# Performance work log

Measured on AMD Instinct MI355X. Metric: run time of the kernel, lower is better.

## Reference

```python
import jax, jax.numpy as jnp
import numpy as np

N = 50000      # nodes
E = 800000     # edges (before self-loops)
IN_DIM = 128
HID = 96
PROJ = 64
BN_EPS = 1e-5
L2_EPS = 1e-12


def setup_inputs() -> dict:
    key = jax.random.key(0)
    ks = jax.random.split(key, 8)

    def glorot(k, shape):
        fan_in, fan_out = shape
        s = np.sqrt(6.0 / (fan_in + fan_out)).astype(np.float32)
        return jax.random.uniform(k, shape, jnp.float32, -s, s)

    x = jax.random.normal(ks[0], (N, IN_DIM), jnp.float32)
    edge_index = jax.random.randint(ks[1], (2, E), 0, N, dtype=jnp.int64)

    return {
        "x": x,
        "edge_index": edge_index,
        # GCN layer 1
        "W1": glorot(ks[2], (IN_DIM, HID)), "b1": jnp.zeros(HID, jnp.float32),
        "g1": jnp.ones(HID, jnp.float32), "be1": jnp.zeros(HID, jnp.float32),
        # GCN layer 2
        "W2": glorot(ks[3], (HID, HID)), "b2": jnp.zeros(HID, jnp.float32),
        "g2": jnp.ones(HID, jnp.float32), "be2": jnp.zeros(HID, jnp.float32),
        # projector: Linear -> BN -> ReLU -> Linear
        "Wp1": glorot(ks[4], (HID, HID)), "bp1": jnp.zeros(HID, jnp.float32),
        "gp": jnp.ones(HID, jnp.float32), "bep": jnp.zeros(HID, jnp.float32),
        "Wp2": glorot(ks[5], (HID, PROJ)), "bp2": jnp.zeros(PROJ, jnp.float32),
    }


def _batchnorm(h, gamma, beta):
    # training-mode BatchNorm1d: batch stats, biased variance
    m = h.mean(axis=0)
    v = h.var(axis=0)
    return gamma * (h - m) * jax.lax.rsqrt(v + BN_EPS) + beta


def _gcn_conv(x, W, b, src, dst, deg_inv_sqrt):
    # PyG GCNConv: x @ W, symmetric-normalized scatter-add (self-loops included
    # in src/dst), then bias.
    xw = x @ W                                              # [N, out]
    norm = deg_inv_sqrt[src] * deg_inv_sqrt[dst]            # [E+N]
    msg = xw[src] * norm[:, None]                           # [E+N, out]
    out = jax.ops.segment_sum(msg, dst, num_segments=x.shape[0])
    return out + b


def reference(x, edge_index, W1, b1, g1, be1, W2, b2, g2, be2,
              Wp1, bp1, gp, bep, Wp2, bp2):
    n = x.shape[0]
    loops = jnp.arange(n, dtype=edge_index.dtype)
    src = jnp.concatenate([edge_index[0], loops])
    dst = jnp.concatenate([edge_index[1], loops])
    deg = jax.ops.segment_sum(jnp.ones(src.shape[0], x.dtype), dst,
                              num_segments=n)               # includes self-loops
    deg_inv_sqrt = jax.lax.rsqrt(deg)                       # deg >= 1 always

    h = jax.nn.relu(_batchnorm(_gcn_conv(x, W1, b1, src, dst, deg_inv_sqrt), g1, be1))
    h = jax.nn.relu(_batchnorm(_gcn_conv(h, W2, b2, src, dst, deg_inv_sqrt), g2, be2))

    z = jax.nn.relu(_batchnorm(h @ Wp1 + bp1, gp, bep))
    z = z @ Wp2 + bp2
    # F.normalize(p=2, dim=-1, eps=1e-12)
    nrm = jnp.linalg.norm(z, axis=-1, keepdims=True)
    return z / jnp.maximum(nrm, L2_EPS)
```

## Files before the change

kernel.cpp:

```cpp
#include <hip/hip_runtime.h>
#include <hip/hip_fp16.h>

constexpr int BLK = 256;

static inline int cdiv(long long a, int b) { return (int)((a + b - 1) / b); }

using v8h = __attribute__((ext_vector_type(8))) _Float16;
using v4f = __attribute__((ext_vector_type(4))) float;


__global__ void count_dst_off(const int* __restrict__ dst, int* __restrict__ cnt,
                              unsigned short* __restrict__ eoff, int E) {
    for (int i = blockIdx.x * blockDim.x + threadIdx.x; i < E; i += gridDim.x * blockDim.x)
        eoff[i] = (unsigned short)atomicAdd(&cnt[dst[i]], 1);
}

__global__ __launch_bounds__(256) void scan1_dis(const int* __restrict__ cnt,
                                                 int* __restrict__ rowptr,
                                                 int* __restrict__ bsum,
                                                 float* __restrict__ dis, int N) {
    __shared__ int ts[256];
    int tid = threadIdx.x;
    int base = blockIdx.x * 1024 + tid * 4;
    int v[4], s = 0;
#pragma unroll
    for (int i = 0; i < 4; ++i) {
        v[i] = (base + i < N) ? cnt[base + i] : 0;
        s += v[i];
        if (base + i < N) dis[base + i] = rsqrtf((float)v[i] + 1.0f);
    }
    ts[tid] = s;
    __syncthreads();
    for (int off = 1; off < 256; off <<= 1) {
        int t = 0;
        if (tid >= off) t = ts[tid - off];
        __syncthreads();
        if (tid >= off) ts[tid] += t;
        __syncthreads();
    }
    int run = ts[tid] - s;
#pragma unroll
    for (int i = 0; i < 4; ++i) {
        if (base + i < N) rowptr[base + i] = run;
        run += v[i];
    }
    if (tid == 255) bsum[blockIdx.x] = ts[255];
}

__global__ __launch_bounds__(256) void scan23(int* __restrict__ rowptr,
                                              const int* __restrict__ bsum,
                                              int nb, int N, int E) {
    __shared__ int sboff[64];
    const int tid = threadIdx.x;
    if (tid < 64) {
        int orig = (tid < nb) ? bsum[tid] : 0;
        int v = orig;
#pragma unroll
        for (int off = 1; off < 64; off <<= 1) {
            int t = __shfl_up(v, off, 64);
            if (tid >= off) v += t;
        }
        sboff[tid] = v - orig;
    }
    __syncthreads();
    int i = blockIdx.x * 256 + tid;
    if (i < N) rowptr[i] += sboff[i >> 10];
    if (i == 0) rowptr[N] = E;
}

__global__ void csr_fill(const int* __restrict__ src, const int* __restrict__ dst,
                         const unsigned short* __restrict__ eoff,
                         const int* __restrict__ rowptr,
                         unsigned short* __restrict__ csrc, int E) {
    for (int i = blockIdx.x * blockDim.x + threadIdx.x; i < E; i += gridDim.x * blockDim.x) {
        csrc[rowptr[dst[i]] + (int)eoff[i]] = (unsigned short)src[i];
    }
}


template <int K, bool ACT, bool BIAS, bool HOUT, bool WOUT, bool STATS>
__device__ __forceinline__ void gemm96_body(int bid,
                                            const float* __restrict__ in,
                                            const float* __restrict__ W,
                                            const float* __restrict__ bias,
                                            const float* __restrict__ bnsums,
                                            const float* __restrict__ gamma,
                                            const float* __restrict__ beta,
                                            const float* __restrict__ dsc,
                                            float* __restrict__ out,
                                            _Float16* __restrict__ hout,
                                            float* __restrict__ osums, int N) {
    constexpr int NK = K / 32;
    constexpr int LDK = K + 8;
    __shared__ __align__(16) _Float16 Wt[96 * LDK];
    __shared__ __align__(16) float ssl[ACT ? 192 : 1];
    __shared__ float sb[STATS ? 192 : 1];
    const int tid = threadIdx.x;
    for (int idx = tid; idx < K * 96; idx += 256) {
        int k = idx / 96, n = idx - k * 96;
        Wt[n * LDK + k] = (_Float16)W[idx];
    }
    if (ACT && tid < 96) {
        float inv_n = 1.0f / (float)N;
        float mean = bnsums[tid] * inv_n;
        float var = bnsums[96 + tid] * inv_n - mean * mean;
        float sc = gamma[tid] * rsqrtf(var + 1e-5f);
        ssl[tid] = sc;
        ssl[96 + tid] = beta[tid] - mean * sc;
    }
    if (STATS && tid < 192) sb[tid] = 0.0f;
    __syncthreads();

    const int wave = tid >> 6, lane = tid & 63;
    const int quad = lane >> 4, lm = lane & 15;
    const int rbase = bid * 64 + wave * 16;
    int arow = rbase + lm;
    arow = arow < N ? arow : N - 1;

    v8h afr[NK];
#pragma unroll
    for (int kc = 0; kc < NK; ++kc) {
        const float* p = &in[(long long)arow * K + kc * 32 + quad * 8];
        float4 p0 = *(const float4*)p;
        float4 p1 = *(const float4*)(p + 4);
        if (ACT) {
            int kk = kc * 32 + quad * 8;
            float4 sc0 = *(const float4*)&ssl[kk];
            float4 sc1 = *(const float4*)&ssl[kk + 4];
            float4 sh0 = *(const float4*)&ssl[96 + kk];
            float4 sh1 = *(const float4*)&ssl[96 + kk + 4];
            p0.x = fmaxf(fmaf(p0.x, sc0.x, sh0.x), 0.0f);
            p0.y = fmaxf(fmaf(p0.y, sc0.y, sh0.y), 0.0f);
            p0.z = fmaxf(fmaf(p0.z, sc0.z, sh0.z), 0.0f);
            p0.w = fmaxf(fmaf(p0.w, sc0.w, sh0.w), 0.0f);
            p1.x = fmaxf(fmaf(p1.x, sc1.x, sh1.x), 0.0f);
            p1.y = fmaxf(fmaf(p1.y, sc1.y, sh1.y), 0.0f);
            p1.z = fmaxf(fmaf(p1.z, sc1.z, sh1.z), 0.0f);
            p1.w = fmaxf(fmaf(p1.w, sc1.w, sh1.w), 0.0f);
        }
        v8h a;
        a[0] = (_Float16)p0.x; a[1] = (_Float16)p0.y;
        a[2] = (_Float16)p0.z; a[3] = (_Float16)p0.w;
        a[4] = (_Float16)p1.x; a[5] = (_Float16)p1.y;
        a[6] = (_Float16)p1.z; a[7] = (_Float16)p1.w;
        afr[kc] = a;
    }

    v4f acc[6];
#pragma unroll
    for (int t = 0; t < 6; ++t) {
        v4f c = {0.0f, 0.0f, 0.0f, 0.0f};
#pragma unroll
        for (int kc = 0; kc < NK; ++kc) {
            v8h b = *(const v8h*)&Wt[(t * 16 + lm) * LDK + kc * 32 + quad * 8];
            c = __builtin_amdgcn_mfma_f32_16x16x32_f16(afr[kc], b, c, 0, 0, 0);
        }
        acc[t] = c;
    }

    float dr[4];
    if (HOUT) {
#pragma unroll
        for (int r = 0; r < 4; ++r) {
            int gr = rbase + quad * 4 + r;
            dr[r] = dsc ? dsc[gr < N ? gr : N - 1] : 1.0f;
        }
    }

    float ls[6], lq[6];
#pragma unroll
    for (int t = 0; t < 6; ++t) { ls[t] = 0.0f; lq[t] = 0.0f; }
#pragma unroll
    for (int t = 0; t < 6; ++t) {
        float bv = BIAS ? bias[t * 16 + lm] : 0.0f;
#pragma unroll
        for (int r = 0; r < 4; ++r) {
            int gr = rbase + quad * 4 + r;
            if (gr < N) {
                float o = acc[t][r] + bv;
                if (WOUT) out[(long long)gr * 96 + t * 16 + lm] = o;
                if (HOUT) hout[(long long)gr * 96 + t * 16 + lm] = (_Float16)(o * dr[r]);
                if (STATS) { ls[t] += o; lq[t] += o * o; }
            }
        }
    }
    if (STATS) {
#pragma unroll
        for (int t = 0; t < 6; ++t) {
            ls[t] += __shfl_xor(ls[t], 16);
            ls[t] += __shfl_xor(ls[t], 32);
            lq[t] += __shfl_xor(lq[t], 16);
            lq[t] += __shfl_xor(lq[t], 32);
        }
        if (quad == 0) {
#pragma unroll
            for (int t = 0; t < 6; ++t) {
                atomicAdd(&sb[t * 16 + lm], ls[t]);
                atomicAdd(&sb[96 + t * 16 + lm], lq[t]);
            }
        }
        __syncthreads();
        if (tid < 192) atomicAdd(&osums[tid], sb[tid]);
    }
}

template <int K, bool ACT, bool BIAS, bool HOUT, bool WOUT, bool STATS>
__global__ __launch_bounds__(256) void gemm96m(const float* __restrict__ in,
                                               const float* __restrict__ W,
                                               const float* __restrict__ bias,
                                               const float* __restrict__ bnsums,
                                               const float* __restrict__ gamma,
                                               const float* __restrict__ beta,
                                               const float* __restrict__ dsc,
                                               float* __restrict__ out,
                                               _Float16* __restrict__ hout,
                                               float* __restrict__ osums, int N) {
    gemm96_body<K, ACT, BIAS, HOUT, WOUT, STATS>(blockIdx.x, in, W, bias, bnsums,
                                                 gamma, beta, dsc, out, hout, osums, N);
}

__global__ __launch_bounds__(256) void gemm1_zero(const float* __restrict__ x,
                                                  const float* __restrict__ W1,
                                                  _Float16* __restrict__ hout,
                                                  int* __restrict__ cnt,
                                                  float* __restrict__ sums,
                                                  int gG, int N) {
    if ((int)blockIdx.x < gG) {
        gemm96_body<128, false, false, true, false, false>(
            blockIdx.x, x, W1, nullptr, nullptr, nullptr, nullptr, nullptr,
            nullptr, hout, nullptr, N);
    } else {
        int g = (blockIdx.x - gG) * 256 + threadIdx.x;
        int stride = (gridDim.x - gG) * 256;
        for (int i = g; i < N; i += stride) cnt[i] = 0;
        if (g < 576) sums[g] = 0.0f;
    }
}


__global__ __launch_bounds__(256) void gemm_finalm(const float* __restrict__ in,
                                                   const float* __restrict__ W,
                                                   const float* __restrict__ bias,
                                                   const float* __restrict__ bnsums,
                                                   const float* __restrict__ gamma,
                                                   const float* __restrict__ beta,
                                                   float* __restrict__ out, int N) {
    constexpr int K = 96, NK = 3, LDK = K + 8;
    __shared__ __align__(16) _Float16 Wt[64 * LDK];
    __shared__ __align__(16) float ssl[192];
    const int tid = threadIdx.x;
    for (int idx = tid; idx < K * 64; idx += 256) {
        int k = idx / 64, n = idx - k * 64;
        Wt[n * LDK + k] = (_Float16)W[idx];
    }
    if (tid < 96) {
        float inv_n = 1.0f / (float)N;
        float mean = bnsums[tid] * inv_n;
        float var = bnsums[96 + tid] * inv_n - mean * mean;
        float sc = gamma[tid] * rsqrtf(var + 1e-5f);
        ssl[tid] = sc;
        ssl[96 + tid] = beta[tid] - mean * sc;
    }
    __syncthreads();

    const int wave = tid >> 6, lane = tid & 63;
    const int quad = lane >> 4, lm = lane & 15;
    const int rbase = blockIdx.x * 64 + wave * 16;
    int arow = rbase + lm;
    arow = arow < N ? arow : N - 1;

    v8h afr[NK];
#pragma unroll
    for (int kc = 0; kc < NK; ++kc) {
        const float* p = &in[(long long)arow * K + kc * 32 + quad * 8];
        float4 p0 = *(const float4*)p;
        float4 p1 = *(const float4*)(p + 4);
        int kk = kc * 32 + quad * 8;
        float4 sc0 = *(const float4*)&ssl[kk];
        float4 sc1 = *(const float4*)&ssl[kk + 4];
        float4 sh0 = *(const float4*)&ssl[96 + kk];
        float4 sh1 = *(const float4*)&ssl[96 + kk + 4];
        p0.x = fmaxf(fmaf(p0.x, sc0.x, sh0.x), 0.0f);
        p0.y = fmaxf(fmaf(p0.y, sc0.y, sh0.y), 0.0f);
        p0.z = fmaxf(fmaf(p0.z, sc0.z, sh0.z), 0.0f);
        p0.w = fmaxf(fmaf(p0.w, sc0.w, sh0.w), 0.0f);
        p1.x = fmaxf(fmaf(p1.x, sc1.x, sh1.x), 0.0f);
        p1.y = fmaxf(fmaf(p1.y, sc1.y, sh1.y), 0.0f);
        p1.z = fmaxf(fmaf(p1.z, sc1.z, sh1.z), 0.0f);
        p1.w = fmaxf(fmaf(p1.w, sc1.w, sh1.w), 0.0f);
        v8h a;
        a[0] = (_Float16)p0.x; a[1] = (_Float16)p0.y;
        a[2] = (_Float16)p0.z; a[3] = (_Float16)p0.w;
        a[4] = (_Float16)p1.x; a[5] = (_Float16)p1.y;
        a[6] = (_Float16)p1.z; a[7] = (_Float16)p1.w;
        afr[kc] = a;
    }

    v4f acc[4];
#pragma unroll
    for (int t = 0; t < 4; ++t) {
        v4f c = {0.0f, 0.0f, 0.0f, 0.0f};
#pragma unroll
        for (int kc = 0; kc < NK; ++kc) {
            v8h b = *(const v8h*)&Wt[(t * 16 + lm) * LDK + kc * 32 + quad * 8];
            c = __builtin_amdgcn_mfma_f32_16x16x32_f16(afr[kc], b, c, 0, 0, 0);
        }
        float bv = bias[t * 16 + lm];
        c[0] += bv; c[1] += bv; c[2] += bv; c[3] += bv;
        acc[t] = c;
    }

    float sq[4];
#pragma unroll
    for (int r = 0; r < 4; ++r) {
        float s = acc[0][r] * acc[0][r] + acc[1][r] * acc[1][r] +
                  acc[2][r] * acc[2][r] + acc[3][r] * acc[3][r];
#pragma unroll
        for (int m = 1; m < 16; m <<= 1) s += __shfl_xor(s, m, 64);
        sq[r] = 1.0f / fmaxf(sqrtf(s), 1e-12f);
    }
#pragma unroll
    for (int r = 0; r < 4; ++r) {
        int gr = rbase + quad * 4 + r;
        if (gr < N) {
#pragma unroll
            for (int t = 0; t < 4; ++t)
                out[(long long)gr * 64 + t * 16 + lm] = acc[t][r] * sq[r];
        }
    }
}


__device__ __forceinline__ void acc_row(float* acc, const __half2* h) {
#pragma unroll
    for (int k = 0; k < 4; ++k) {
        float2 f = __half22float2(h[k]);
        acc[2 * k + 0] += f.x;
        acc[2 * k + 1] += f.y;
    }
}

__device__ __forceinline__ void acc_roww(float* acc, const __half2* h, float w) {
#pragma unroll
    for (int k = 0; k < 4; ++k) {
        float2 f = __half22float2(h[k]);
        acc[2 * k + 0] = fmaf(f.x, w, acc[2 * k + 0]);
        acc[2 * k + 1] = fmaf(f.y, w, acc[2 * k + 1]);
    }
}

template <bool PRESC>
__global__ __launch_bounds__(256) void agg96h(const __half* __restrict__ hxw,
                                              const int* __restrict__ rowptr,
                                              const unsigned short* __restrict__ csrc,
                                              const float* __restrict__ dis,
                                              const float* __restrict__ bias,
                                              float* __restrict__ out, int N) {
    int idx = blockIdx.x * 256 + threadIdx.x;
    if (idx >= N * 12) return;
    int n = idx / 12, c8 = idx % 12;
    int ch = c8 * 8;
    float dn = dis[n];
    float acc[8];
    {
        float sw = PRESC ? 1.0f : dn;
        float4 g = *(const float4*)&hxw[(long long)n * 96 + ch];
        const __half2* hs = (const __half2*)&g;
#pragma unroll
        for (int k = 0; k < 4; ++k) {
            float2 f = __half22float2(hs[k]);
            acc[2 * k + 0] = f.x * sw;
            acc[2 * k + 1] = f.y * sw;
        }
    }
    int e = rowptr[n], e1 = rowptr[n + 1];
    for (; e + 7 < e1; e += 8) {
        int s[8];
        float4 g[8];
        float w[8];
#pragma unroll
        for (int j = 0; j < 8; ++j) s[j] = csrc[e + j];
        if (!PRESC) {
#pragma unroll
            for (int j = 0; j < 8; ++j) w[j] = dis[s[j]];
        }
#pragma unroll
        for (int j = 0; j < 8; ++j)
            g[j] = *(const float4*)&hxw[(long long)s[j] * 96 + ch];
#pragma unroll
        for (int j = 0; j < 8; ++j) {
            if (PRESC) acc_row(acc, (const __half2*)&g[j]);
            else       acc_roww(acc, (const __half2*)&g[j], w[j]);
        }
    }
    for (; e + 3 < e1; e += 4) {
        int s[4];
        float4 g[4];
        float w[4];
#pragma unroll
        for (int j = 0; j < 4; ++j) s[j] = csrc[e + j];
        if (!PRESC) {
#pragma unroll
            for (int j = 0; j < 4; ++j) w[j] = dis[s[j]];
        }
#pragma unroll
        for (int j = 0; j < 4; ++j)
            g[j] = *(const float4*)&hxw[(long long)s[j] * 96 + ch];
#pragma unroll
        for (int j = 0; j < 4; ++j) {
            if (PRESC) acc_row(acc, (const __half2*)&g[j]);
            else       acc_roww(acc, (const __half2*)&g[j], w[j]);
        }
    }
    for (; e < e1; ++e) {
        int s0 = csrc[e];
        float4 g0 = *(const float4*)&hxw[(long long)s0 * 96 + ch];
        if (PRESC) acc_row(acc, (const __half2*)&g0);
        else       acc_roww(acc, (const __half2*)&g0, dis[s0]);
    }
    float4 o0, o1;
    o0.x = fmaf(acc[0], dn, bias[ch + 0]);
    o0.y = fmaf(acc[1], dn, bias[ch + 1]);
    o0.z = fmaf(acc[2], dn, bias[ch + 2]);
    o0.w = fmaf(acc[3], dn, bias[ch + 3]);
    o1.x = fmaf(acc[4], dn, bias[ch + 4]);
    o1.y = fmaf(acc[5], dn, bias[ch + 5]);
    o1.z = fmaf(acc[6], dn, bias[ch + 6]);
    o1.w = fmaf(acc[7], dn, bias[ch + 7]);
    *(float4*)&out[(long long)n * 96 + ch] = o0;
    *(float4*)&out[(long long)n * 96 + ch + 4] = o1;
}


__global__ __launch_bounds__(256) void bn_stats96(const float* __restrict__ h,
                                                  float* __restrict__ sums, int N) {
    __shared__ float sb[192];
    const int tid = threadIdx.x;
    if (tid < 192) sb[tid] = 0.0f;
    __syncthreads();
    int g = blockIdx.x * 256 + tid;
    int total = N * 24, stride = gridDim.x * 256;
    float4 s4 = {0, 0, 0, 0}, q4 = {0, 0, 0, 0};
    int c4 = g % 24;
    for (int i = g; i < total; i += stride) {
        int n = i / 24;
        float4 v = *(const float4*)&h[n * 96 + 4 * c4];
        s4.x += v.x; s4.y += v.y; s4.z += v.z; s4.w += v.w;
        q4.x += v.x * v.x; q4.y += v.y * v.y; q4.z += v.z * v.z; q4.w += v.w * v.w;
    }
    atomicAdd(&sb[4 * c4 + 0], s4.x);
    atomicAdd(&sb[4 * c4 + 1], s4.y);
    atomicAdd(&sb[4 * c4 + 2], s4.z);
    atomicAdd(&sb[4 * c4 + 3], s4.w);
    atomicAdd(&sb[96 + 4 * c4 + 0], q4.x);
    atomicAdd(&sb[96 + 4 * c4 + 1], q4.y);
    atomicAdd(&sb[96 + 4 * c4 + 2], q4.z);
    atomicAdd(&sb[96 + 4 * c4 + 3], q4.w);
    __syncthreads();
    if (tid < 192) atomicAdd(&sums[tid], sb[tid]);
}


extern "C" void kernel_launch(void* const* d_in, const int* in_sizes, int n_in,
                              void* d_out, int out_size, void* d_ws, size_t ws_size,
                              hipStream_t stream) {
    const float* x   = (const float*)d_in[0];
    const int*   ei  = (const int*)d_in[1];
    const float* W1  = (const float*)d_in[2];
    const float* b1  = (const float*)d_in[3];
    const float* g1  = (const float*)d_in[4];
    const float* be1 = (const float*)d_in[5];
    const float* W2  = (const float*)d_in[6];
    const float* b2  = (const float*)d_in[7];
    const float* g2  = (const float*)d_in[8];
    const float* be2 = (const float*)d_in[9];
    const float* Wp1 = (const float*)d_in[10];
    const float* bp1 = (const float*)d_in[11];
    const float* gp  = (const float*)d_in[12];
    const float* bep = (const float*)d_in[13];
    const float* Wp2 = (const float*)d_in[14];
    const float* bp2 = (const float*)d_in[15];

    const int N = in_sizes[0] / 128;
    const int E = in_sizes[1] / 2;
    const int* src = ei;
    const int* dst = ei + E;

    char* w = (char*)d_ws;
    auto alloc = [&](size_t bytes) { char* p = w; w += (bytes + 15) & ~size_t(15); return p; };
    int*            cnt    = (int*)alloc((size_t)N * 4);
    int*            rowptr = (int*)alloc((size_t)(N + 1) * 4);
    int*            bsum   = (int*)alloc(64 * 4);
    float*          dis    = (float*)alloc((size_t)N * 4);
    unsigned short* eoff   = (unsigned short*)alloc((size_t)E * 2);
    unsigned short* csrc   = (unsigned short*)alloc((size_t)E * 2);
    float*          buf1   = (float*)alloc((size_t)N * 96 * 4);
    float*          buf2   = (float*)alloc((size_t)N * 96 * 4);
    _Float16*       hbuf   = (_Float16*)alloc((size_t)N * 96 * 2);
    float*          sums   = (float*)alloc(576 * 4);
    float* sums1 = sums, *sums2 = sums + 192, *sums3 = sums + 384;

    float* out = (float*)d_out;

    const int gE  = cdiv(E, BLK);
    const int gG  = cdiv(N, 64);
    const int gA  = cdiv((long long)N * 12, BLK);
    const int nb  = cdiv(N, 1024);

    gemm1_zero<<<gG + nb, 256, 0, stream>>>(x, W1, hbuf, cnt, sums, gG, N);
    count_dst_off<<<gE, BLK, 0, stream>>>(dst, cnt, eoff, E);
    scan1_dis<<<nb, 256, 0, stream>>>(cnt, rowptr, bsum, dis, N);
    scan23<<<cdiv(N, 256), 256, 0, stream>>>(rowptr, bsum, nb, N, E);
    csr_fill<<<gE, BLK, 0, stream>>>(src, dst, eoff, rowptr, csrc, E);

    agg96h<false><<<gA, 256, 0, stream>>>((const __half*)hbuf, rowptr, csrc, dis,
                                          b1, buf2, N);
    bn_stats96<<<510, 256, 0, stream>>>(buf2, sums1, N);

    gemm96m<96, true, false, true, false, false><<<gG, 256, 0, stream>>>(
        buf2, W2, nullptr, sums1, g1, be1, dis, nullptr, hbuf, nullptr, N);
    agg96h<true><<<gA, 256, 0, stream>>>((const __half*)hbuf, rowptr, csrc, dis,
                                         b2, buf2, N);
    bn_stats96<<<510, 256, 0, stream>>>(buf2, sums2, N);

    gemm96m<96, true, true, false, true, true><<<gG, 256, 0, stream>>>(
        buf2, Wp1, bp1, sums2, g2, be2, nullptr, buf1, nullptr, sums3, N);

    gemm_finalm<<<gG, 256, 0, stream>>>(buf1, Wp2, bp2, sums3, gp, bep, out, N);
}
```

Measured before the change: 333.7 us.

## Store intermediate activations in fp16 and fuse degree counting into first GEMM

Aggregation outputs, BN statistics inputs and the projector hidden activations are now kept in fp16 instead of fp32, halving their memory traffic across several kernels. The separate edge-counting kernel is merged into the first GEMM launch as extra blocks, and zeroing of counters and sums moves to a single memset. In exchange, BN statistics are computed from fp16-rounded values and the pre-BN projector output is stored in fp16, which adds rounding error.

```diff
diff --git a/kernel.cpp b/kernel.cpp
--- a/kernel.cpp
+++ b/kernel.cpp
@@ -8,12 +8,6 @@
 using v8h = __attribute__((ext_vector_type(8))) _Float16;
 using v4f = __attribute__((ext_vector_type(4))) float;
 
-
-__global__ void count_dst_off(const int* __restrict__ dst, int* __restrict__ cnt,
-                              unsigned short* __restrict__ eoff, int E) {
-    for (int i = blockIdx.x * blockDim.x + threadIdx.x; i < E; i += gridDim.x * blockDim.x)
-        eoff[i] = (unsigned short)atomicAdd(&cnt[dst[i]], 1);
-}
 
 __global__ __launch_bounds__(256) void scan1_dis(const int* __restrict__ cnt,
                                                  int* __restrict__ rowptr,
@@ -78,16 +72,15 @@
 }
 
 
-template <int K, bool ACT, bool BIAS, bool HOUT, bool WOUT, bool STATS>
+template <int K, bool ACT, bool BIAS, bool STATS, typename TIN>
 __device__ __forceinline__ void gemm96_body(int bid,
-                                            const float* __restrict__ in,
+                                            const TIN* __restrict__ in,
                                             const float* __restrict__ W,
                                             const float* __restrict__ bias,
                                             const float* __restrict__ bnsums,
                                             const float* __restrict__ gamma,
                                             const float* __restrict__ beta,
                                             const float* __restrict__ dsc,
-                                            float* __restrict__ out,
                                             _Float16* __restrict__ hout,
                                             float* __restrict__ osums, int N) {
     constexpr int NK = K / 32;
@@ -120,30 +113,43 @@
     v8h afr[NK];
 #pragma unroll
     for (int kc = 0; kc < NK; ++kc) {
-        const float* p = &in[(long long)arow * K + kc * 32 + quad * 8];
-        float4 p0 = *(const float4*)p;
-        float4 p1 = *(const float4*)(p + 4);
-        if (ACT) {
-            int kk = kc * 32 + quad * 8;
-            float4 sc0 = *(const float4*)&ssl[kk];
-            float4 sc1 = *(const float4*)&ssl[kk + 4];
-            float4 sh0 = *(const float4*)&ssl[96 + kk];
-            float4 sh1 = *(const float4*)&ssl[96 + kk + 4];
-            p0.x = fmaxf(fmaf(p0.x, sc0.x, sh0.x), 0.0f);
-            p0.y = fmaxf(fmaf(p0.y, sc0.y, sh0.y), 0.0f);
-            p0.z = fmaxf(fmaf(p0.z, sc0.z, sh0.z), 0.0f);
-            p0.w = fmaxf(fmaf(p0.w, sc0.w, sh0.w), 0.0f);
-            p1.x = fmaxf(fmaf(p1.x, sc1.x, sh1.x), 0.0f);
-            p1.y = fmaxf(fmaf(p1.y, sc1.y, sh1.y), 0.0f);
-            p1.z = fmaxf(fmaf(p1.z, sc1.z, sh1.z), 0.0f);
-            p1.w = fmaxf(fmaf(p1.w, sc1.w, sh1.w), 0.0f);
-        }
-        v8h a;
-        a[0] = (_Float16)p0.x; a[1] = (_Float16)p0.y;
-        a[2] = (_Float16)p0.z; a[3] = (_Float16)p0.w;
-        a[4] = (_Float16)p1.x; a[5] = (_Float16)p1.y;
-        a[6] = (_Float16)p1.z; a[7] = (_Float16)p1.w;
-        afr[kc] = a;
+        const int kk = kc * 32 + quad * 8;
+        if constexpr (sizeof(TIN) == 4) {
+            const float* p = (const float*)&in[(long long)arow * K + kk];
+            float4 p0 = *(const float4*)p;
+            float4 p1 = *(const float4*)(p + 4);
+            if (ACT) {
+                float4 sc0 = *(const float4*)&ssl[kk];
+                float4 sc1 = *(const float4*)&ssl[kk + 4];
+                float4 sh0 = *(const float4*)&ssl[96 + kk];
+                float4 sh1 = *(const float4*)&ssl[96 + kk + 4];
+                p0.x = fmaxf(fmaf(p0.x, sc0.x, sh0.x), 0.0f);
+                p0.y = fmaxf(fmaf(p0.y, sc0.y, sh0.y), 0.0f);
+                p0.z = fmaxf(fmaf(p0.z, sc0.z, sh0.z), 0.0f);
+                p0.w = fmaxf(fmaf(p0.w, sc0.w, sh0.w), 0.0f);
+                p1.x = fmaxf(fmaf(p1.x, sc1.x, sh1.x), 0.0f);
+                p1.y = fmaxf(fmaf(p1.y, sc1.y, sh1.y), 0.0f);
+                p1.z = fmaxf(fmaf(p1.z, sc1.z, sh1.z), 0.0f);
+                p1.w = fmaxf(fmaf(p1.w, sc1.w, sh1.w), 0.0f);
+            }
+            v8h a;
+            a[0] = (_Float16)p0.x; a[1] = (_Float16)p0.y;
+            a[2] = (_Float16)p0.z; a[3] = (_Float16)p0.w;
+            a[4] = (_Float16)p1.x; a[5] = (_Float16)p1.y;
+            a[6] = (_Float16)p1.z; a[7] = (_Float16)p1.w;
+            afr[kc] = a;
+        } else {
+            v8h hv = *(const v8h*)&in[(long long)arow * K + kk];
+            if (ACT) {
+#pragma unroll
+                for (int j = 0; j < 8; ++j) {
+                    float f = (float)hv[j];
+                    f = fmaxf(fmaf(f, ssl[kk + j], ssl[96 + kk + j]), 0.0f);
+                    hv[j] = (_Float16)f;
+                }
+            }
+            afr[kc] = hv;
+        }
     }
 
     v4f acc[6];
@@ -159,12 +165,10 @@
     }
 
     float dr[4];
-    if (HOUT) {
-#pragma unroll
-        for (int r = 0; r < 4; ++r) {
-            int gr = rbase + quad * 4 + r;
-            dr[r] = dsc ? dsc[gr < N ? gr : N - 1] : 1.0f;
-        }
+#pragma unroll
+    for (int r = 0; r < 4; ++r) {
+        int gr = rbase + quad * 4 + r;
+        dr[r] = dsc ? dsc[gr < N ? gr : N - 1] : 1.0f;
     }
 
     float ls[6], lq[6];
@@ -178,8 +182,7 @@
             int gr = rbase + quad * 4 + r;
             if (gr < N) {
                 float o = acc[t][r] + bv;
-                if (WOUT) out[(long long)gr * 96 + t * 16 + lm] = o;
-                if (HOUT) hout[(long long)gr * 96 + t * 16 + lm] = (_Float16)(o * dr[r]);
+                hout[(long long)gr * 96 + t * 16 + lm] = (_Float16)(o * dr[r]);
                 if (STATS) { ls[t] += o; lq[t] += o * o; }
             }
         }
@@ -204,41 +207,41 @@
     }
 }
 
-template <int K, bool ACT, bool BIAS, bool HOUT, bool WOUT, bool STATS>
-__global__ __launch_bounds__(256) void gemm96m(const float* __restrict__ in,
+template <int K, bool ACT, bool BIAS, bool STATS, typename TIN>
+__global__ __launch_bounds__(256) void gemm96m(const TIN* __restrict__ in,
                                                const float* __restrict__ W,
                                                const float* __restrict__ bias,
                                                const float* __restrict__ bnsums,
                                                const float* __restrict__ gamma,
                                                const float* __restrict__ beta,
                                                const float* __restrict__ dsc,
-                                               float* __restrict__ out,
                                                _Float16* __restrict__ hout,
                                                float* __restrict__ osums, int N) {
-    gemm96_body<K, ACT, BIAS, HOUT, WOUT, STATS>(blockIdx.x, in, W, bias, bnsums,
-                                                 gamma, beta, dsc, out, hout, osums, N);
-}
-
-__global__ __launch_bounds__(256) void gemm1_zero(const float* __restrict__ x,
-                                                  const float* __restrict__ W1,
-                                                  _Float16* __restrict__ hout,
-                                                  int* __restrict__ cnt,
-                                                  float* __restrict__ sums,
-                                                  int gG, int N) {
+    gemm96_body<K, ACT, BIAS, STATS, TIN>(blockIdx.x, in, W, bias, bnsums,
+                                          gamma, beta, dsc, hout, osums, N);
+}
+
+__global__ __launch_bounds__(256) void gemm1_count(const float* __restrict__ x,
+                                                   const float* __restrict__ W1,
+                                                   _Float16* __restrict__ hout,
+                                                   const int* __restrict__ dst,
+                                                   int* __restrict__ cnt,
+                                                   unsigned short* __restrict__ eoff,
+                                                   int gG, int N, int E) {
     if ((int)blockIdx.x < gG) {
-        gemm96_body<128, false, false, true, false, false>(
+        gemm96_body<128, false, false, false, float>(
             blockIdx.x, x, W1, nullptr, nullptr, nullptr, nullptr, nullptr,
-            nullptr, hout, nullptr, N);
+            hout, nullptr, N);
     } else {
         int g = (blockIdx.x - gG) * 256 + threadIdx.x;
         int stride = (gridDim.x - gG) * 256;
-        for (int i = g; i < N; i += stride) cnt[i] = 0;
-        if (g < 576) sums[g] = 0.0f;
-    }
-}
-
-
-__global__ __launch_bounds__(256) void gemm_finalm(const float* __restrict__ in,
+        for (int i = g; i < E; i += stride)
+            eoff[i] = (unsigned short)atomicAdd(&cnt[dst[i]], 1);
+    }
+}
+
+
+__global__ __launch_bounds__(256) void gemm_finalm(const _Float16* __restrict__ in,
                                                    const float* __restrict__ W,
                                                    const float* __restrict__ bias,
                                                    const float* __restrict__ bnsums,
@@ -272,28 +275,15 @@
     v8h afr[NK];
 #pragma unroll
     for (int kc = 0; kc < NK; ++kc) {
-        const float* p = &in[(long long)arow * K + kc * 32 + quad * 8];
-        float4 p0 = *(const float4*)p;
-        float4 p1 = *(const float4*)(p + 4);
-        int kk = kc * 32 + quad * 8;
-        float4 sc0 = *(const float4*)&ssl[kk];
-        float4 sc1 = *(const float4*)&ssl[kk + 4];
-        float4 sh0 = *(const float4*)&ssl[96 + kk];
-        float4 sh1 = *(const float4*)&ssl[96 + kk + 4];
-        p0.x = fmaxf(fmaf(p0.x, sc0.x, sh0.x), 0.0f);
-        p0.y = fmaxf(fmaf(p0.y, sc0.y, sh0.y), 0.0f);
-        p0.z = fmaxf(fmaf(p0.z, sc0.z, sh0.z), 0.0f);
-        p0.w = fmaxf(fmaf(p0.w, sc0.w, sh0.w), 0.0f);
-        p1.x = fmaxf(fmaf(p1.x, sc1.x, sh1.x), 0.0f);
-        p1.y = fmaxf(fmaf(p1.y, sc1.y, sh1.y), 0.0f);
-        p1.z = fmaxf(fmaf(p1.z, sc1.z, sh1.z), 0.0f);
-        p1.w = fmaxf(fmaf(p1.w, sc1.w, sh1.w), 0.0f);
-        v8h a;
-        a[0] = (_Float16)p0.x; a[1] = (_Float16)p0.y;
-        a[2] = (_Float16)p0.z; a[3] = (_Float16)p0.w;
-        a[4] = (_Float16)p1.x; a[5] = (_Float16)p1.y;
-        a[6] = (_Float16)p1.z; a[7] = (_Float16)p1.w;
-        afr[kc] = a;
+        const int kk = kc * 32 + quad * 8;
+        v8h hv = *(const v8h*)&in[(long long)arow * K + kk];
+#pragma unroll
+        for (int j = 0; j < 8; ++j) {
+            float f = (float)hv[j];
+            f = fmaxf(fmaf(f, ssl[kk + j], ssl[96 + kk + j]), 0.0f);
+            hv[j] = (_Float16)f;
+        }
+        afr[kc] = hv;
     }
 
     v4f acc[4];
@@ -355,7 +345,7 @@
                                               const unsigned short* __restrict__ csrc,
                                               const float* __restrict__ dis,
                                               const float* __restrict__ bias,
-                                              float* __restrict__ out, int N) {
+                                              _Float16* __restrict__ outh, int N) {
     int idx = blockIdx.x * 256 + threadIdx.x;
     if (idx >= N * 12) return;
     int n = idx / 12, c8 = idx % 12;
@@ -418,44 +408,43 @@
         if (PRESC) acc_row(acc, (const __half2*)&g0);
         else       acc_roww(acc, (const __half2*)&g0, dis[s0]);
     }
-    float4 o0, o1;
-    o0.x = fmaf(acc[0], dn, bias[ch + 0]);
-    o0.y = fmaf(acc[1], dn, bias[ch + 1]);
-    o0.z = fmaf(acc[2], dn, bias[ch + 2]);
-    o0.w = fmaf(acc[3], dn, bias[ch + 3]);
-    o1.x = fmaf(acc[4], dn, bias[ch + 4]);
-    o1.y = fmaf(acc[5], dn, bias[ch + 5]);
-    o1.z = fmaf(acc[6], dn, bias[ch + 6]);
-    o1.w = fmaf(acc[7], dn, bias[ch + 7]);
-    *(float4*)&out[(long long)n * 96 + ch] = o0;
-    *(float4*)&out[(long long)n * 96 + ch + 4] = o1;
-}
-
-
-__global__ __launch_bounds__(256) void bn_stats96(const float* __restrict__ h,
-                                                  float* __restrict__ sums, int N) {
+    v8h o;
+#pragma unroll
+    for (int j = 0; j < 8; ++j)
+        o[j] = (_Float16)fmaf(acc[j], dn, bias[ch + j]);
+    *(v8h*)&outh[(long long)n * 96 + ch] = o;
+}
+
+
+__global__ __launch_bounds__(256) void bn_stats96h(const __half* __restrict__ h,
+                                                   float* __restrict__ sums, int N) {
     __shared__ float sb[192];
     const int tid = threadIdx.x;
     if (tid < 192) sb[tid] = 0.0f;
     __syncthreads();
     int g = blockIdx.x * 256 + tid;
-    int total = N * 24, stride = gridDim.x * 256;
-    float4 s4 = {0, 0, 0, 0}, q4 = {0, 0, 0, 0};
-    int c4 = g % 24;
+    int total = N * 12, stride = gridDim.x * 256;
+    int c8 = g % 12;
+    float s[8] = {0, 0, 0, 0, 0, 0, 0, 0};
+    float q[8] = {0, 0, 0, 0, 0, 0, 0, 0};
     for (int i = g; i < total; i += stride) {
-        int n = i / 24;
-        float4 v = *(const float4*)&h[n * 96 + 4 * c4];
-        s4.x += v.x; s4.y += v.y; s4.z += v.z; s4.w += v.w;
-        q4.x += v.x * v.x; q4.y += v.y * v.y; q4.z += v.z * v.z; q4.w += v.w * v.w;
-    }
-    atomicAdd(&sb[4 * c4 + 0], s4.x);
-    atomicAdd(&sb[4 * c4 + 1], s4.y);
-    atomicAdd(&sb[4 * c4 + 2], s4.z);
-    atomicAdd(&sb[4 * c4 + 3], s4.w);
-    atomicAdd(&sb[96 + 4 * c4 + 0], q4.x);
-    atomicAdd(&sb[96 + 4 * c4 + 1], q4.y);
-    atomicAdd(&sb[96 + 4 * c4 + 2], q4.z);
-    atomicAdd(&sb[96 + 4 * c4 + 3], q4.w);
+        int n = i / 12;
+        float4 raw = *(const float4*)&h[n * 96 + 8 * c8];
+        const __half2* hp = (const __half2*)&raw;
+#pragma unroll
+        for (int k = 0; k < 4; ++k) {
+            float2 f = __half22float2(hp[k]);
+            s[2 * k + 0] += f.x;
+            s[2 * k + 1] += f.y;
+            q[2 * k + 0] += f.x * f.x;
+            q[2 * k + 1] += f.y * f.y;
+        }
+    }
+#pragma unroll
+    for (int j = 0; j < 8; ++j) {
+        atomicAdd(&sb[8 * c8 + j], s[j]);
+        atomicAdd(&sb[96 + 8 * c8 + j], q[j]);
+    }
     __syncthreads();
     if (tid < 192) atomicAdd(&sums[tid], sb[tid]);
 }
@@ -489,42 +478,44 @@
     char* w = (char*)d_ws;
     auto alloc = [&](size_t bytes) { char* p = w; w += (bytes + 15) & ~size_t(15); return p; };
     int*            cnt    = (int*)alloc((size_t)N * 4);
+    float*          sums   = (float*)alloc(576 * 4);
     int*            rowptr = (int*)alloc((size_t)(N + 1) * 4);
     int*            bsum   = (int*)alloc(64 * 4);
     float*          dis    = (float*)alloc((size_t)N * 4);
     unsigned short* eoff   = (unsigned short*)alloc((size_t)E * 2);
     unsigned short* csrc   = (unsigned short*)alloc((size_t)E * 2);
-    float*          buf1   = (float*)alloc((size_t)N * 96 * 4);
-    float*          buf2   = (float*)alloc((size_t)N * 96 * 4);
+    _Float16*       buf2h  = (_Float16*)alloc((size_t)N * 96 * 2);
     _Float16*       hbuf   = (_Float16*)alloc((size_t)N * 96 * 2);
-    float*          sums   = (float*)alloc(576 * 4);
     float* sums1 = sums, *sums2 = sums + 192, *sums3 = sums + 384;
 
     float* out = (float*)d_out;
 
     const int gE  = cdiv(E, BLK);
     const int gG  = cdiv(N, 64);
+    const int gC  = 1024;
     const int gA  = cdiv((long long)N * 12, BLK);
     const int nb  = cdiv(N, 1024);
 
-    gemm1_zero<<<gG + nb, 256, 0, stream>>>(x, W1, hbuf, cnt, sums, gG, N);
-    count_dst_off<<<gE, BLK, 0, stream>>>(dst, cnt, eoff, E);
+    size_t zlen = (size_t)((char*)sums - (char*)cnt) + 576 * 4;
+    hipMemsetAsync(cnt, 0, zlen, stream);
+
+    gemm1_count<<<gG + gC, 256, 0, stream>>>(x, W1, hbuf, dst, cnt, eoff, gG, N, E);
     scan1_dis<<<nb, 256, 0, stream>>>(cnt, rowptr, bsum, dis, N);
     scan23<<<cdiv(N, 256), 256, 0, stream>>>(rowptr, bsum, nb, N, E);
     csr_fill<<<gE, BLK, 0, stream>>>(src, dst, eoff, rowptr, csrc, E);
 
     agg96h<false><<<gA, 256, 0, stream>>>((const __half*)hbuf, rowptr, csrc, dis,
-                                          b1, buf2, N);
-    bn_stats96<<<510, 256, 0, stream>>>(buf2, sums1, N);
-
-    gemm96m<96, true, false, true, false, false><<<gG, 256, 0, stream>>>(
-        buf2, W2, nullptr, sums1, g1, be1, dis, nullptr, hbuf, nullptr, N);
+                                          b1, buf2h, N);
+    bn_stats96h<<<510, 256, 0, stream>>>((const __half*)buf2h, sums1, N);
+
+    gemm96m<96, true, false, false, _Float16><<<gG, 256, 0, stream>>>(
+        buf2h, W2, nullptr, sums1, g1, be1, dis, hbuf, nullptr, N);
     agg96h<true><<<gA, 256, 0, stream>>>((const __half*)hbuf, rowptr, csrc, dis,
-                                         b2, buf2, N);
-    bn_stats96<<<510, 256, 0, stream>>>(buf2, sums2, N);
-
-    gemm96m<96, true, true, false, true, true><<<gG, 256, 0, stream>>>(
-        buf2, Wp1, bp1, sums2, g2, be2, nullptr, buf1, nullptr, sums3, N);
-
-    gemm_finalm<<<gG, 256, 0, stream>>>(buf1, Wp2, bp2, sums3, gp, bep, out, N);
-}
+                                         b2, buf2h, N);
+    bn_stats96h<<<510, 256, 0, stream>>>((const __half*)buf2h, sums2, N);
+
+    gemm96m<96, true, true, true, _Float16><<<gG, 256, 0, stream>>>(
+        buf2h, Wp1, bp1, sums2, g2, be2, nullptr, hbuf, sums3, N);
+
+    gemm_finalm<<<gG, 256, 0, stream>>>(hbuf, Wp2, bp2, sums3, gp, bep, out, N);
+}
```

Measured after the change: 308.2 us. -7.7%, faster.
